# Performance work log

Measured on AMD Instinct MI355X. Metric: run time of the kernel, lower is better.

Reference implementation:

```python
import jax, jax.numpy as jnp
import numpy as np

NEG_SLOPE = 0.01  # torch nn.LeakyReLU default


def setup_inputs() -> dict:
    key = jax.random.key(0)
    k1, k2, k3, k4, k5 = jax.random.split(key, 5)
    B, C, N, O = 32, 512, 1024, 512
    x = jax.random.normal(k1, (B, C, N), dtype=jnp.float32)
    wq = jax.random.normal(k2, (C,), dtype=jnp.float32) * (1.0 / np.sqrt(C))
    wk = jax.random.normal(k3, (C,), dtype=jnp.float32) * (1.0 / np.sqrt(C))
    wm = jax.random.normal(k4, (O, C), dtype=jnp.float32) * (1.0 / np.sqrt(C))
    bm = jax.random.normal(k5, (O,), dtype=jnp.float32) * 0.01
    return {"x": x, "wq": wq, "wk": wk, "wm": wm, "bm": bm}


def reference(x, wq, wk, wm, bm):
    # x: [B, C, N]
    q = jnp.einsum('c,bcn->bn', wq, x)            # [B, N] (Conv1d C->1, k=1, no bias)
    k = jnp.einsum('c,bcn->bn', wk, x)            # [B, N]
    scores = q[:, None, :] + k[:, :, None]        # [B, N, N] additive broadcast
    scores = jnp.where(scores > 0, scores, NEG_SLOPE * scores)  # LeakyReLU
    att = jax.nn.softmax(scores, axis=-1)         # softmax over last dim
    agg = jnp.einsum('bcn,bmn->bcm', x, att)      # weighted aggregation [B, C, N]
    out = jnp.einsum('oc,bcm->bom', wm, agg) + bm[None, :, None]  # Conv1d k=1
    return jax.nn.relu(out)
```

## Files before the change

kernel.cpp:

```cpp
#include <hip/hip_runtime.h>


constexpr int B = 32, C = 512, N = 1024, O = 512;
constexpr float L2E = 1.4426950408889634f;

typedef _Float16 half8 __attribute__((ext_vector_type(8)));
typedef _Float16 half4v __attribute__((ext_vector_type(4)));
typedef _Float16 half2v __attribute__((ext_vector_type(2)));
typedef float f32x4 __attribute__((ext_vector_type(4)));

#if __has_builtin(__builtin_amdgcn_exp2f)
#define EXP2(x) __builtin_amdgcn_exp2f(x)
#else
#define EXP2(x) exp2f(x)
#endif

__device__ __forceinline__ half8 cvt8(float4 a, float4 b) {
  half8 h;
  h[0] = (_Float16)a.x; h[1] = (_Float16)a.y; h[2] = (_Float16)a.z; h[3] = (_Float16)a.w;
  h[4] = (_Float16)b.x; h[5] = (_Float16)b.y; h[6] = (_Float16)b.z; h[7] = (_Float16)b.w;
  return h;
}

__global__ __launch_bounds__(256) void gemm_y_kernel(const float* __restrict__ x,
    const float* __restrict__ wm, const float* __restrict__ wq,
    const float* __restrict__ wk, float* __restrict__ q, float* __restrict__ k,
    _Float16* __restrict__ Yt) {
  __shared__ half2v Xs[16 * 130];
  __shared__ __align__(16) _Float16 Ws[128 * 40];
  int b  = blockIdx.y;
  int n0 = blockIdx.x * 128;
  int o0 = blockIdx.z * 128;
  int t = threadIdx.x;
  int w = t >> 6, l = t & 63;
  int nw = w >> 1, ow = w & 1;
  int lm = l & 15, q8 = (l >> 4) * 8, q4 = (l >> 4) * 4;

  int cp = t >> 4, ng = t & 15;
  int wrow = t >> 2, woff = (t & 3) * 8;
  bool doqk = (blockIdx.z == 0);
  float aq[8] = {}, ak[8] = {};

  f32x4 acc[4][4] = {};
  for (int c0 = 0; c0 < C; c0 += 32) {
    const float* xr = x + ((size_t)b * C + c0 + 2 * cp) * N + n0 + ng * 8;
    float4 a0 = *(const float4*)(xr);
    float4 a1 = *(const float4*)(xr + 4);
    float4 b0 = *(const float4*)(xr + N);
    float4 b1 = *(const float4*)(xr + N + 4);
    const float* wr = wm + (size_t)(o0 + wrow) * C + c0 + woff;
    float4 w0 = *(const float4*)(wr);
    float4 w1 = *(const float4*)(wr + 4);
    float4 w2 = *(const float4*)(wr + (size_t)64 * C);
    float4 w3 = *(const float4*)(wr + (size_t)64 * C + 4);

    if (doqk) {
      float2 wq2 = *(const float2*)&wq[c0 + 2 * cp];
      float2 wk2 = *(const float2*)&wk[c0 + 2 * cp];
      aq[0] = fmaf(wq2.x, a0.x, fmaf(wq2.y, b0.x, aq[0]));
      aq[1] = fmaf(wq2.x, a0.y, fmaf(wq2.y, b0.y, aq[1]));
      aq[2] = fmaf(wq2.x, a0.z, fmaf(wq2.y, b0.z, aq[2]));
      aq[3] = fmaf(wq2.x, a0.w, fmaf(wq2.y, b0.w, aq[3]));
      aq[4] = fmaf(wq2.x, a1.x, fmaf(wq2.y, b1.x, aq[4]));
      aq[5] = fmaf(wq2.x, a1.y, fmaf(wq2.y, b1.y, aq[5]));
      aq[6] = fmaf(wq2.x, a1.z, fmaf(wq2.y, b1.z, aq[6]));
      aq[7] = fmaf(wq2.x, a1.w, fmaf(wq2.y, b1.w, aq[7]));
      ak[0] = fmaf(wk2.x, a0.x, fmaf(wk2.y, b0.x, ak[0]));
      ak[1] = fmaf(wk2.x, a0.y, fmaf(wk2.y, b0.y, ak[1]));
      ak[2] = fmaf(wk2.x, a0.z, fmaf(wk2.y, b0.z, ak[2]));
      ak[3] = fmaf(wk2.x, a0.w, fmaf(wk2.y, b0.w, ak[3]));
      ak[4] = fmaf(wk2.x, a1.x, fmaf(wk2.y, b1.x, ak[4]));
      ak[5] = fmaf(wk2.x, a1.y, fmaf(wk2.y, b1.y, ak[5]));
      ak[6] = fmaf(wk2.x, a1.z, fmaf(wk2.y, b1.z, ak[6]));
      ak[7] = fmaf(wk2.x, a1.w, fmaf(wk2.y, b1.w, ak[7]));
    }

    __syncthreads();
    {
      half2v* xp = &Xs[cp * 130 + ng * 8];
      xp[0] = half2v{(_Float16)a0.x, (_Float16)b0.x};
      xp[1] = half2v{(_Float16)a0.y, (_Float16)b0.y};
      xp[2] = half2v{(_Float16)a0.z, (_Float16)b0.z};
      xp[3] = half2v{(_Float16)a0.w, (_Float16)b0.w};
      xp[4] = half2v{(_Float16)a1.x, (_Float16)b1.x};
      xp[5] = half2v{(_Float16)a1.y, (_Float16)b1.y};
      xp[6] = half2v{(_Float16)a1.z, (_Float16)b1.z};
      xp[7] = half2v{(_Float16)a1.w, (_Float16)b1.w};
      *(half8*)&Ws[wrow * 40 + woff]        = cvt8(w0, w1);
      *(half8*)&Ws[(wrow + 64) * 40 + woff] = cvt8(w2, w3);
    }
    __syncthreads();

    half8 af[4], bf[4];
#pragma unroll
    for (int i = 0; i < 4; ++i) {
      int nrow = nw * 64 + i * 16 + lm;
#pragma unroll
      for (int jp = 0; jp < 4; ++jp) {
        half2v p = Xs[(q4 + jp) * 130 + nrow];
        af[i][2 * jp]     = p[0];
        af[i][2 * jp + 1] = p[1];
      }
    }
#pragma unroll
    for (int j = 0; j < 4; ++j)
      bf[j] = *(const half8*)&Ws[(ow * 64 + j * 16 + lm) * 40 + q8];
#pragma unroll
    for (int i = 0; i < 4; ++i)
#pragma unroll
      for (int j = 0; j < 4; ++j)
        acc[i][j] = __builtin_amdgcn_mfma_f32_16x16x32_f16(af[i], bf[j], acc[i][j], 0, 0, 0);
  }

#pragma unroll
  for (int i = 0; i < 4; ++i) {
    int n_b = n0 + nw * 64 + i * 16 + (l >> 4) * 4;
#pragma unroll
    for (int j = 0; j < 4; ++j) {
      int o_c = o0 + ow * 64 + j * 16 + lm;
      half4v h;
      h[0] = (_Float16)acc[i][j][0];
      h[1] = (_Float16)acc[i][j][1];
      h[2] = (_Float16)acc[i][j][2];
      h[3] = (_Float16)acc[i][j][3];
      *(half4v*)&Yt[((size_t)b * O + o_c) * N + n_b] = h;
    }
  }

  if (doqk) {
    float* red = (float*)Ws;
    __syncthreads();
#pragma unroll
    for (int j = 0; j < 8; ++j) red[cp * 132 + ng * 8 + j] = aq[j];
    __syncthreads();
    if (t < 128) {
      float s = 0.f;
#pragma unroll
      for (int p = 0; p < 16; ++p) s += red[p * 132 + t];
      q[b * N + n0 + t] = L2E * s;
    }
    __syncthreads();
#pragma unroll
    for (int j = 0; j < 8; ++j) red[cp * 132 + ng * 8 + j] = ak[j];
    __syncthreads();
    if (t < 128) {
      float s = 0.f;
#pragma unroll
      for (int p = 0; p < 16; ++p) s += red[p * 132 + t];
      k[b * N + n0 + t] = L2E * s;
    }
  }
}

__global__ __launch_bounds__(256) void qmax_kernel(const float* __restrict__ q,
                                                   float* __restrict__ qmax) {
  int b = blockIdx.x;
  int tid = threadIdx.x;
  float m = -1e30f;
  for (int n = tid; n < N; n += 256) m = fmaxf(m, q[b * N + n]);
#pragma unroll
  for (int off = 32; off > 0; off >>= 1) m = fmaxf(m, __shfl_down(m, off, 64));
  __shared__ float red[4];
  if ((tid & 63) == 0) red[tid >> 6] = m;
  __syncthreads();
  if (tid == 0) qmax[b] = fmaxf(fmaxf(red[0], red[1]), fmaxf(red[2], red[3]));
}

__global__ __launch_bounds__(256) void gemm_out_kernel(const _Float16* __restrict__ Yt,
    const float* __restrict__ q, const float* __restrict__ k,
    const float* __restrict__ qmax, const float* __restrict__ bm,
    float* __restrict__ out) {
  __shared__ __align__(16) float qs[N];
  __shared__ __align__(16) _Float16 Ys[128 * 40];
  __shared__ float izs[128];
  int b  = blockIdx.y;
  int o0 = blockIdx.x * 128;
  int m0 = blockIdx.z * 128;
  int t = threadIdx.x;
  int w = t >> 6, l = t & 63;
  int lm = l & 15, g = l >> 4, q8 = g * 8;

  *(float4*)&qs[t * 4] = *(const float4*)&q[b * N + t * 4];

  float qmv = qmax[b];
  float k2[2], k3[2];
#pragma unroll
  for (int i = 0; i < 2; ++i) {
    float km = k[b * N + m0 + w * 32 + i * 16 + lm];
    float s0 = qmv + km;
    float M  = fmaxf(s0, 0.01f * s0);
    k2[i] = km - M;
    k3[i] = fmaf(0.01f, km, -M);
  }
  float Zp[2] = {0.f, 0.f};
  int yr = t >> 1, yp = t & 1;
  const _Float16* ysrc = Yt + ((size_t)b * O + o0 + yr) * N + yp * 16;
  __syncthreads();

  f32x4 acc[2][8] = {};
  for (int n0k = 0; n0k < N; n0k += 32) {
    half8 y0 = *(const half8*)(ysrc + n0k);
    half8 y1 = *(const half8*)(ysrc + n0k + 8);
    float4 qa = *(const float4*)&qs[n0k + q8];
    float4 qb = *(const float4*)&qs[n0k + q8 + 4];
    float qv[8] = {qa.x, qa.y, qa.z, qa.w, qb.x, qb.y, qb.z, qb.w};
    half8 af[2];
#pragma unroll
    for (int i = 0; i < 2; ++i) {
      float zz = 0.f;
#pragma unroll
      for (int jj = 0; jj < 8; ++jj) {
        float arg = fmaxf(qv[jj] + k2[i], fmaf(0.01f, qv[jj], k3[i]));
        _Float16 eh = (_Float16)EXP2(arg);
        af[i][jj] = eh;
        zz += (float)eh;
      }
      Zp[i] += zz;
    }
    __syncthreads();
    *(half8*)&Ys[yr * 40 + yp * 16]     = y0;
    *(half8*)&Ys[yr * 40 + yp * 16 + 8] = y1;
    __syncthreads();

    half8 bf[8];
#pragma unroll
    for (int j = 0; j < 8; ++j)
      bf[j] = *(const half8*)&Ys[(j * 16 + lm) * 40 + q8];
#pragma unroll
    for (int i = 0; i < 2; ++i)
#pragma unroll
      for (int j = 0; j < 8; ++j)
        acc[i][j] = __builtin_amdgcn_mfma_f32_16x16x32_f16(af[i], bf[j], acc[i][j], 0, 0, 0);
  }

#pragma unroll
  for (int i = 0; i < 2; ++i) {
    float z = Zp[i];
    z += __shfl_xor(z, 16, 64);
    z += __shfl_xor(z, 32, 64);
    if (g == 0) izs[w * 32 + i * 16 + lm] = 1.0f / z;
  }
  __syncthreads();

#pragma unroll
  for (int i = 0; i < 2; ++i) {
    int m_b = m0 + w * 32 + i * 16 + g * 4;
    float4 iz4 = *(const float4*)&izs[w * 32 + i * 16 + g * 4];
#pragma unroll
    for (int j = 0; j < 8; ++j) {
      int o_c = o0 + j * 16 + lm;
      float bias = bm[o_c];
      float4 r;
      r.x = fmaxf(fmaf(acc[i][j][0], iz4.x, bias), 0.f);
      r.y = fmaxf(fmaf(acc[i][j][1], iz4.y, bias), 0.f);
      r.z = fmaxf(fmaf(acc[i][j][2], iz4.z, bias), 0.f);
      r.w = fmaxf(fmaf(acc[i][j][3], iz4.w, bias), 0.f);
      *(float4*)&out[((size_t)b * O + o_c) * N + m_b] = r;
    }
  }
}

extern "C" void kernel_launch(void* const* d_in, const int* in_sizes, int n_in,
                              void* d_out, int out_size, void* d_ws, size_t ws_size,
                              hipStream_t stream) {
  const float* x  = (const float*)d_in[0];
  const float* wq = (const float*)d_in[1];
  const float* wk = (const float*)d_in[2];
  const float* wm = (const float*)d_in[3];
  const float* bm = (const float*)d_in[4];
  float* out = (float*)d_out;

  float* q    = (float*)d_ws;
  float* k    = q + B * N;
  float* qmax = k + B * N;
  _Float16* Yt = (_Float16*)(qmax + 64);

  gemm_y_kernel<<<dim3(N / 128, B, O / 128), 256, 0, stream>>>(x, wm, wq, wk, q, k, Yt);
  qmax_kernel<<<dim3(B), 256, 0, stream>>>(q, qmax);
  gemm_out_kernel<<<dim3(O / 128, B, N / 128), 256, 0, stream>>>(Yt, q, k, qmax, bm, out);
}
```

Baseline: 224.0 us.

## Fuse qmax into first GEMM via atomicMax and double-buffer Y tiles

Removes the separate qmax kernel: each z==0 block of the first GEMM reduces its q values and publishes the max with an order-preserving uint atomicMax. The buffer is zeroed by a memset beforehand. The output GEMM now double-buffers the Y tile in shared memory, prefetching the next tile while computing, so each iteration needs one barrier instead of two. The epilogue is also reordered to load the bias once per column. This adds a memset launch and atomics, and it uses more LDS.

Result: no change. 227.3 us (+1.5%).

```diff
diff --git a/kernel.cpp b/kernel.cpp
--- a/kernel.cpp
+++ b/kernel.cpp
@@ -22,12 +22,22 @@
   return h;
 }
 
+__device__ __forceinline__ unsigned fenc(float x) {
+  unsigned u = __float_as_uint(x);
+  return (u & 0x80000000u) ? ~u : (u ^ 0x80000000u);
+}
+__device__ __forceinline__ float fdec(unsigned e) {
+  unsigned u = (e & 0x80000000u) ? (e ^ 0x80000000u) : ~e;
+  return __uint_as_float(u);
+}
+
 __global__ __launch_bounds__(256) void gemm_y_kernel(const float* __restrict__ x,
     const float* __restrict__ wm, const float* __restrict__ wq,
     const float* __restrict__ wk, float* __restrict__ q, float* __restrict__ k,
-    _Float16* __restrict__ Yt) {
+    unsigned* __restrict__ qmax_u, _Float16* __restrict__ Yt) {
   __shared__ half2v Xs[16 * 130];
   __shared__ __align__(16) _Float16 Ws[128 * 40];
+  __shared__ float mred[4];
   int b  = blockIdx.y;
   int n0 = blockIdx.x * 128;
   int o0 = blockIdx.z * 128;
@@ -129,6 +139,7 @@
 
   if (doqk) {
     float* red = (float*)Ws;
+    float qv_final = -1e30f;
     __syncthreads();
 #pragma unroll
     for (int j = 0; j < 8; ++j) red[cp * 132 + ng * 8 + j] = aq[j];
@@ -137,7 +148,8 @@
       float s = 0.f;
 #pragma unroll
       for (int p = 0; p < 16; ++p) s += red[p * 132 + t];
-      q[b * N + n0 + t] = L2E * s;
+      qv_final = L2E * s;
+      q[b * N + n0 + t] = qv_final;
     }
     __syncthreads();
 #pragma unroll
@@ -149,29 +161,24 @@
       for (int p = 0; p < 16; ++p) s += red[p * 132 + t];
       k[b * N + n0 + t] = L2E * s;
     }
-  }
-}
-
-__global__ __launch_bounds__(256) void qmax_kernel(const float* __restrict__ q,
-                                                   float* __restrict__ qmax) {
-  int b = blockIdx.x;
-  int tid = threadIdx.x;
-  float m = -1e30f;
-  for (int n = tid; n < N; n += 256) m = fmaxf(m, q[b * N + n]);
-#pragma unroll
-  for (int off = 32; off > 0; off >>= 1) m = fmaxf(m, __shfl_down(m, off, 64));
-  __shared__ float red[4];
-  if ((tid & 63) == 0) red[tid >> 6] = m;
-  __syncthreads();
-  if (tid == 0) qmax[b] = fmaxf(fmaxf(red[0], red[1]), fmaxf(red[2], red[3]));
+    float m = qv_final;
+#pragma unroll
+    for (int off = 32; off > 0; off >>= 1) m = fmaxf(m, __shfl_down(m, off, 64));
+    if ((t & 63) == 0) mred[t >> 6] = m;
+    __syncthreads();
+    if (t == 0) {
+      float bmax = fmaxf(fmaxf(mred[0], mred[1]), fmaxf(mred[2], mred[3]));
+      atomicMax(&qmax_u[b], fenc(bmax));
+    }
+  }
 }
 
 __global__ __launch_bounds__(256) void gemm_out_kernel(const _Float16* __restrict__ Yt,
     const float* __restrict__ q, const float* __restrict__ k,
-    const float* __restrict__ qmax, const float* __restrict__ bm,
+    const unsigned* __restrict__ qmax_u, const float* __restrict__ bm,
     float* __restrict__ out) {
   __shared__ __align__(16) float qs[N];
-  __shared__ __align__(16) _Float16 Ys[128 * 40];
+  __shared__ __align__(16) _Float16 Ys[2][128 * 40];
   __shared__ float izs[128];
   int b  = blockIdx.y;
   int o0 = blockIdx.x * 128;
@@ -182,7 +189,7 @@
 
   *(float4*)&qs[t * 4] = *(const float4*)&q[b * N + t * 4];
 
-  float qmv = qmax[b];
+  float qmv = fdec(qmax_u[b]);
   float k2[2], k3[2];
 #pragma unroll
   for (int i = 0; i < 2; ++i) {
@@ -195,12 +202,24 @@
   float Zp[2] = {0.f, 0.f};
   int yr = t >> 1, yp = t & 1;
   const _Float16* ysrc = Yt + ((size_t)b * O + o0 + yr) * N + yp * 16;
+
+  {
+    half8 y0 = *(const half8*)(ysrc);
+    half8 y1 = *(const half8*)(ysrc + 8);
+    *(half8*)&Ys[0][yr * 40 + yp * 16]     = y0;
+    *(half8*)&Ys[0][yr * 40 + yp * 16 + 8] = y1;
+  }
   __syncthreads();
 
   f32x4 acc[2][8] = {};
-  for (int n0k = 0; n0k < N; n0k += 32) {
-    half8 y0 = *(const half8*)(ysrc + n0k);
-    half8 y1 = *(const half8*)(ysrc + n0k + 8);
+  for (int it = 0; it < N / 32; ++it) {
+    int p = it & 1;
+    int n0k = it * 32;
+    half8 z0, z1;
+    if (it < N / 32 - 1) {
+      z0 = *(const half8*)(ysrc + n0k + 32);
+      z1 = *(const half8*)(ysrc + n0k + 40);
+    }
     float4 qa = *(const float4*)&qs[n0k + q8];
     float4 qb = *(const float4*)&qs[n0k + q8 + 4];
     float qv[8] = {qa.x, qa.y, qa.z, qa.w, qb.x, qb.y, qb.z, qb.w};
@@ -217,20 +236,20 @@
       }
       Zp[i] += zz;
     }
-    __syncthreads();
-    *(half8*)&Ys[yr * 40 + yp * 16]     = y0;
-    *(half8*)&Ys[yr * 40 + yp * 16 + 8] = y1;
-    __syncthreads();
-
     half8 bf[8];
 #pragma unroll
     for (int j = 0; j < 8; ++j)
-      bf[j] = *(const half8*)&Ys[(j * 16 + lm) * 40 + q8];
+      bf[j] = *(const half8*)&Ys[p][(j * 16 + lm) * 40 + q8];
 #pragma unroll
     for (int i = 0; i < 2; ++i)
 #pragma unroll
       for (int j = 0; j < 8; ++j)
         acc[i][j] = __builtin_amdgcn_mfma_f32_16x16x32_f16(af[i], bf[j], acc[i][j], 0, 0, 0);
+    if (it < N / 32 - 1) {
+      *(half8*)&Ys[p ^ 1][yr * 40 + yp * 16]     = z0;
+      *(half8*)&Ys[p ^ 1][yr * 40 + yp * 16 + 8] = z1;
+    }
+    __syncthreads();
   }
 
 #pragma unroll
@@ -242,19 +261,24 @@
   }
   __syncthreads();
 
+  float iz4v[2][4];
 #pragma unroll
   for (int i = 0; i < 2; ++i) {
-    int m_b = m0 + w * 32 + i * 16 + g * 4;
     float4 iz4 = *(const float4*)&izs[w * 32 + i * 16 + g * 4];
-#pragma unroll
-    for (int j = 0; j < 8; ++j) {
-      int o_c = o0 + j * 16 + lm;
-      float bias = bm[o_c];
+    iz4v[i][0] = iz4.x; iz4v[i][1] = iz4.y; iz4v[i][2] = iz4.z; iz4v[i][3] = iz4.w;
+  }
+#pragma unroll
+  for (int j = 0; j < 8; ++j) {
+    int o_c = o0 + j * 16 + lm;
+    float bias = bm[o_c];
+#pragma unroll
+    for (int i = 0; i < 2; ++i) {
+      int m_b = m0 + w * 32 + i * 16 + g * 4;
       float4 r;
-      r.x = fmaxf(fmaf(acc[i][j][0], iz4.x, bias), 0.f);
-      r.y = fmaxf(fmaf(acc[i][j][1], iz4.y, bias), 0.f);
-      r.z = fmaxf(fmaf(acc[i][j][2], iz4.z, bias), 0.f);
-      r.w = fmaxf(fmaf(acc[i][j][3], iz4.w, bias), 0.f);
+      r.x = fmaxf(fmaf(acc[i][j][0], iz4v[i][0], bias), 0.f);
+      r.y = fmaxf(fmaf(acc[i][j][1], iz4v[i][1], bias), 0.f);
+      r.z = fmaxf(fmaf(acc[i][j][2], iz4v[i][2], bias), 0.f);
+      r.w = fmaxf(fmaf(acc[i][j][3], iz4v[i][3], bias), 0.f);
       *(float4*)&out[((size_t)b * O + o_c) * N + m_b] = r;
     }
   }
@@ -272,10 +296,10 @@
 
   float* q    = (float*)d_ws;
   float* k    = q + B * N;
-  float* qmax = k + B * N;
-  _Float16* Yt = (_Float16*)(qmax + 64);
-
-  gemm_y_kernel<<<dim3(N / 128, B, O / 128), 256, 0, stream>>>(x, wm, wq, wk, q, k, Yt);
-  qmax_kernel<<<dim3(B), 256, 0, stream>>>(q, qmax);
-  gemm_out_kernel<<<dim3(O / 128, B, N / 128), 256, 0, stream>>>(Yt, q, k, qmax, bm, out);
-}
+  unsigned* qmax_u = (unsigned*)(k + B * N);
+  _Float16* Yt = (_Float16*)(qmax_u + 64);
+
+  hipMemsetAsync(qmax_u, 0, 64 * sizeof(unsigned), stream);
+  gemm_y_kernel<<<dim3(N / 128, B, O / 128), 256, 0, stream>>>(x, wm, wq, wk, q, k, qmax_u, Yt);
+  gemm_out_kernel<<<dim3(O / 128, B, N / 128), 256, 0, stream>>>(Yt, q, k, qmax_u, bm, out);
+}
```
